# Optimization experiments

Measured on AMD Instinct MI355X. Metric: run time of the kernel, lower is better.

The kernel has to match this reference:

```python
import jax, jax.numpy as jnp
import numpy as np

NUM_HEADS = 6
H_SP, W_SP = 8, 16
LN_EPS = 1e-5


def _ln(x, g, b):
    m = x.mean(-1, keepdims=True)
    v = ((x - m) ** 2).mean(-1, keepdims=True)
    return (x - m) / jnp.sqrt(v + LN_EPS) * g + b


def setup_inputs():
    key = jax.random.key(0)
    ks = jax.random.split(key, 8)
    B, H, W, C = 8, 128, 128, 192
    L = H * W
    N = H_SP * W_SP
    nW = L // N
    pos_dim = C // 16  # (dim//4)//4 = 12
    qkv = jax.random.normal(ks[0], (3, B, L, C), jnp.float32)
    mask = jax.random.normal(ks[1], (nW, N, N), jnp.float32) * 0.1

    def lin(k, i, o):
        return jax.random.normal(k, (i, o), jnp.float32) * 0.02

    pos_dimv = pos_dim
    pos_proj_w = lin(ks[2], 2, pos_dimv); pos_proj_b = jnp.zeros((pos_dimv,), jnp.float32)
    ln1_g = jnp.ones((pos_dimv,), jnp.float32); ln1_b = jnp.zeros((pos_dimv,), jnp.float32)
    lin1_w = lin(ks[3], pos_dimv, pos_dimv); lin1_b = jnp.zeros((pos_dimv,), jnp.float32)
    ln2_g = jnp.ones((pos_dimv,), jnp.float32); ln2_b = jnp.zeros((pos_dimv,), jnp.float32)
    lin2_w = lin(ks[4], pos_dimv, pos_dimv); lin2_b = jnp.zeros((pos_dimv,), jnp.float32)
    ln3_g = jnp.ones((pos_dimv,), jnp.float32); ln3_b = jnp.zeros((pos_dimv,), jnp.float32)
    lin3_w = lin(ks[5], pos_dimv, NUM_HEADS); lin3_b = jnp.zeros((NUM_HEADS,), jnp.float32)
    # buffers: rpe_biases [(2Hsp-1)*(2Wsp-1), 2], relative_position_index [N, N]
    ph = np.arange(1 - H_SP, H_SP); pw = np.arange(1 - W_SP, W_SP)
    biases = np.stack(np.meshgrid(ph, pw, indexing='ij')).reshape(2, -1).T.astype(np.float32)
    coords = np.stack(np.meshgrid(np.arange(H_SP), np.arange(W_SP), indexing='ij')).reshape(2, -1)
    rel = (coords[:, :, None] - coords[:, None, :]).transpose(1, 2, 0).copy()
    rel[..., 0] += H_SP - 1
    rel[..., 1] += W_SP - 1
    rel[..., 0] *= 2 * W_SP - 1
    rel_idx = rel.sum(-1).astype(np.int32)
    return dict(qkv=qkv, mask=mask, pos_proj_w=pos_proj_w, pos_proj_b=pos_proj_b,
                ln1_g=ln1_g, ln1_b=ln1_b, lin1_w=lin1_w, lin1_b=lin1_b,
                ln2_g=ln2_g, ln2_b=ln2_b, lin2_w=lin2_w, lin2_b=lin2_b,
                ln3_g=ln3_g, ln3_b=ln3_b, lin3_w=lin3_w, lin3_b=lin3_b,
                rpe_biases=jnp.asarray(biases), rel_idx=jnp.asarray(rel_idx), H=H, W=W)


def reference(qkv, mask, pos_proj_w, pos_proj_b, ln1_g, ln1_b, lin1_w, lin1_b,
              ln2_g, ln2_b, lin2_w, lin2_b, ln3_g, ln3_b, lin3_w, lin3_b,
              rpe_biases, rel_idx, H, W):
    q, k, v = qkv[0], qkv[1], qkv[2]
    B, L, C = q.shape
    hd = C // NUM_HEADS
    scale = hd ** -0.5
    N = H_SP * W_SP
    nW = H * W // N
    # pooled query: adaptive avg-pool on first half channels, max-pool on second half
    q_img = q.transpose(0, 2, 1).reshape(B, C, H, W)
    half = C // 2
    blocks = lambda t: t.reshape(B, -1, H_SP, H // H_SP, W_SP, W // W_SP)
    q1 = blocks(q_img[:, :half]).mean(axis=(3, 5))   # [B, C/2, Hsp, Wsp]
    q2 = blocks(q_img[:, half:]).max(axis=(3, 5))
    qp = jnp.concatenate([q1, q2], 1).reshape(B, NUM_HEADS, hd, N).transpose(0, 1, 3, 2)
    qw = jnp.tile(qp, (nW, 1, 1, 1)) * scale  # [B*nW, h, N, d]  (torch .repeat ordering)

    def im2win(x):  # [B, L, C] -> [B*nW, h, N, d]
        xi = x.transpose(0, 2, 1).reshape(B, C, H // H_SP, H_SP, W // W_SP, W_SP)
        xi = xi.transpose(0, 2, 4, 3, 5, 1).reshape(-1, N, C)
        return xi.reshape(-1, N, NUM_HEADS, hd).transpose(0, 2, 1, 3)

    kw, vw = im2win(k), im2win(v)
    attn = jnp.einsum('whqd,whkd->whqk', qw, kw)  # [B*nW, h, N, N]
    # DynamicPosBias MLP on relative coordinates, gathered into scores
    pos = rpe_biases @ pos_proj_w + pos_proj_b
    pos = jax.nn.relu(_ln(pos, ln1_g, ln1_b)) @ lin1_w + lin1_b
    pos = jax.nn.relu(_ln(pos, ln2_g, ln2_b)) @ lin2_w + lin2_b
    pos = jax.nn.relu(_ln(pos, ln3_g, ln3_b)) @ lin3_w + lin3_b  # [M, heads]
    rpb = pos[rel_idx]  # [N, N, heads]
    attn = attn + rpb.transpose(2, 0, 1)[None]
    attn = attn.reshape(B, nW, NUM_HEADS, N, N) + mask[None, :, None]
    attn = jax.nn.softmax(attn.reshape(-1, NUM_HEADS, N, N), axis=-1)
    x = jnp.einsum('whqk,whkd->whqd', attn, vw).transpose(0, 2, 1, 3).reshape(-1, N, C)
    # windows2img
    out = x.reshape(B, H // H_SP, W // W_SP, H_SP, W_SP, C)
    out = out.transpose(0, 1, 3, 2, 4, 5).reshape(B, H, W, C)
    return out
```

## Files before the change

kernel.cpp:

```cpp
#include <hip/hip_runtime.h>
#include <cstdint>
#include <cstddef>

typedef __attribute__((ext_vector_type(8))) short short8;
typedef __attribute__((ext_vector_type(4))) float f32x4;

#define SCALE 0.17677669529663687f
#define KOFF 25165824UL
#define VOFF 50331648UL

__device__ __forceinline__ float bf2f(unsigned short u){
  union { unsigned int i; float f; } x; x.i = ((unsigned int)u) << 16; return x.f;
}
__device__ __forceinline__ unsigned short f2bf(float f){
  union { float f; unsigned int i; } x; x.f = f;
  unsigned int u = x.i;
  unsigned int r = u + 0x7fffu + ((u >> 16) & 1u);
  return (unsigned short)(r >> 16);
}

__device__ __forceinline__ int detect_bf16(const void* probe){
  const unsigned short* p = (const unsigned short*)probe;
  int ok = 1;
  #pragma unroll
  for (int i = 0; i < 32; i++){
    unsigned short u = p[2*i];
    int e = (u >> 7) & 0xFF;
    ok &= (e >= 0x60 && e <= 0x90) ? 1 : 0;
  }
  return ok;
}

__device__ __forceinline__ float ld1(const void* p, size_t i, int isbf){
  return isbf ? bf2f(((const unsigned short*)p)[i]) : ((const float*)p)[i];
}
__device__ __forceinline__ short8 ld8(const void* p, size_t i, int isbf){
  short8 r;
  if (isbf){
    r = *(const short8*)((const unsigned short*)p + i);
  } else {
    const float4* f = (const float4*)((const float*)p + i);
    float4 u0 = f[0], u1 = f[1];
    r[0] = (short)f2bf(u0.x); r[1] = (short)f2bf(u0.y);
    r[2] = (short)f2bf(u0.z); r[3] = (short)f2bf(u0.w);
    r[4] = (short)f2bf(u1.x); r[5] = (short)f2bf(u1.y);
    r[6] = (short)f2bf(u1.z); r[7] = (short)f2bf(u1.w);
  }
  return r;
}
__device__ __forceinline__ float4 ld4(const void* p, size_t i, int isbf){
  if (!isbf) return *(const float4*)((const float*)p + i);
  const unsigned short* u = (const unsigned short*)p + i;
  uint2 w = *(const uint2*)u;
  float4 r;
  r.x = bf2f((unsigned short)(w.x & 0xffffu)); r.y = bf2f((unsigned short)(w.x >> 16));
  r.z = bf2f((unsigned short)(w.y & 0xffffu)); r.w = bf2f((unsigned short)(w.y >> 16));
  return r;
}

__global__ void posmlp_kernel(const void* __restrict__ probe,
    const void* __restrict__ rpe,
    const void* __restrict__ w0, const void* __restrict__ b0,
    const void* __restrict__ g1, const void* __restrict__ be1,
    const void* __restrict__ w1, const void* __restrict__ bb1,
    const void* __restrict__ g2, const void* __restrict__ be2,
    const void* __restrict__ w2, const void* __restrict__ bb2,
    const void* __restrict__ g3, const void* __restrict__ be3,
    const void* __restrict__ w3, const void* __restrict__ bb3,
    float* __restrict__ pos_table)
{
  const int isbf = detect_bf16(probe);
  int r = blockIdx.x * blockDim.x + threadIdx.x;
  if (r >= 465) return;
  float x0 = ld1(rpe, 2*r, isbf), x1 = ld1(rpe, 2*r+1, isbf);
  float h[12], y[12];
  #pragma unroll
  for (int j=0;j<12;j++) h[j] = x0*ld1(w0,j,isbf) + x1*ld1(w0,12+j,isbf) + ld1(b0,j,isbf);

  {
    float m=0.f;
    #pragma unroll
    for (int j=0;j<12;j++) m += h[j];
    m *= (1.f/12.f);
    float v=0.f;
    #pragma unroll
    for (int j=0;j<12;j++){ float d=h[j]-m; v += d*d; }
    v *= (1.f/12.f);
    float rs = 1.0f/sqrtf(v + 1e-5f);
    #pragma unroll
    for (int j=0;j<12;j++) y[j] = fmaxf((h[j]-m)*rs*ld1(g1,j,isbf) + ld1(be1,j,isbf), 0.f);
    #pragma unroll
    for (int j=0;j<12;j++){
      float s = ld1(bb1,j,isbf);
      #pragma unroll
      for (int i=0;i<12;i++) s += y[i]*ld1(w1,i*12+j,isbf);
      h[j] = s;
    }
  }
  {
    float m=0.f;
    #pragma unroll
    for (int j=0;j<12;j++) m += h[j];
    m *= (1.f/12.f);
    float v=0.f;
    #pragma unroll
    for (int j=0;j<12;j++){ float d=h[j]-m; v += d*d; }
    v *= (1.f/12.f);
    float rs = 1.0f/sqrtf(v + 1e-5f);
    #pragma unroll
    for (int j=0;j<12;j++) y[j] = fmaxf((h[j]-m)*rs*ld1(g2,j,isbf) + ld1(be2,j,isbf), 0.f);
    #pragma unroll
    for (int j=0;j<12;j++){
      float s = ld1(bb2,j,isbf);
      #pragma unroll
      for (int i=0;i<12;i++) s += y[i]*ld1(w2,i*12+j,isbf);
      h[j] = s;
    }
  }
  {
    float m=0.f;
    #pragma unroll
    for (int j=0;j<12;j++) m += h[j];
    m *= (1.f/12.f);
    float v=0.f;
    #pragma unroll
    for (int j=0;j<12;j++){ float d=h[j]-m; v += d*d; }
    v *= (1.f/12.f);
    float rs = 1.0f/sqrtf(v + 1e-5f);
    #pragma unroll
    for (int j=0;j<12;j++) y[j] = fmaxf((h[j]-m)*rs*ld1(g3,j,isbf) + ld1(be3,j,isbf), 0.f);
    #pragma unroll
    for (int o=0;o<6;o++){
      float s = ld1(bb3,o,isbf);
      #pragma unroll
      for (int i=0;i<12;i++) s += y[i]*ld1(w3,i*6+o,isbf);
      pos_table[r*6+o] = s;
    }
  }
}

__global__ void gatherN_kernel(const int* __restrict__ rel_idx,
                               const float* __restrict__ pos_table,
                               unsigned short* __restrict__ rpbN)
{
  const int idx = blockIdx.x * 256 + threadIdx.x;
  const int h = blockIdx.y;
  rpbN[h*16384 + idx] = f2bf(pos_table[rel_idx[idx]*6 + h]);
}

__global__ void pool_kernel(const void* __restrict__ qkv,
                            unsigned short* __restrict__ poolq)
{
  const int isbf = detect_bf16(qkv);
  const int b = blockIdx.y;
  const int n = blockIdx.x;
  const int t = threadIdx.x;
  const int cg = t % 48, sub = t / 48;
  const int ph = n >> 4, pw = n & 15;
  const size_t cell = ((size_t)(b*16384 + ph*16*128 + pw*8))*192 + cg*4;
  const bool avg = (cg < 24);
  float4 acc;
  if (avg){ acc.x=0.f; acc.y=0.f; acc.z=0.f; acc.w=0.f; }
  else    { acc.x=-3.4e38f; acc.y=-3.4e38f; acc.z=-3.4e38f; acc.w=-3.4e38f; }
  #pragma unroll
  for (int hh=0; hh<4; hh++){
    const int hi = sub*4 + hh;
    #pragma unroll
    for (int wi=0; wi<8; wi++){
      float4 xv = ld4(qkv, cell + (size_t)(hi*128 + wi)*192, isbf);
      if (avg){ acc.x+=xv.x; acc.y+=xv.y; acc.z+=xv.z; acc.w+=xv.w; }
      else { acc.x=fmaxf(acc.x,xv.x); acc.y=fmaxf(acc.y,xv.y);
             acc.z=fmaxf(acc.z,xv.z); acc.w=fmaxf(acc.w,xv.w); }
    }
  }
  __shared__ float4 pr[4][48];
  pr[sub][cg] = acc;
  __syncthreads();
  if (sub == 0){
    #pragma unroll
    for (int s=1; s<4; s++){
      float4 xv = pr[s][cg];
      if (avg){ acc.x+=xv.x; acc.y+=xv.y; acc.z+=xv.z; acc.w+=xv.w; }
      else { acc.x=fmaxf(acc.x,xv.x); acc.y=fmaxf(acc.y,xv.y);
             acc.z=fmaxf(acc.z,xv.z); acc.w=fmaxf(acc.w,xv.w); }
    }
    if (avg){ acc.x*=(1.f/128.f); acc.y*=(1.f/128.f); acc.z*=(1.f/128.f); acc.w*=(1.f/128.f); }
    unsigned int lo = (unsigned int)f2bf(acc.x*SCALE) | ((unsigned int)f2bf(acc.y*SCALE) << 16);
    unsigned int hi = (unsigned int)f2bf(acc.z*SCALE) | ((unsigned int)f2bf(acc.w*SCALE) << 16);
    uint2 st; st.x = lo; st.y = hi;
    *(uint2*)(poolq + ((size_t)b*128 + n)*192 + cg*4) = st;
  }
}

__global__ __launch_bounds__(256, 4)
void attn_kernel(const void* __restrict__ qkv,
                 const unsigned short* __restrict__ poolq,
                 const void* __restrict__ mask,
                 const unsigned short* __restrict__ rpbN,
                 void* __restrict__ out)
{
  const int isbf = detect_bf16(qkv);
  const int iw = blockIdx.x, b = blockIdx.y, head = blockIdx.z;
  const int hb = iw >> 3, wb = iw & 7;
  const int qb = iw & 7;
  const int tid = threadIdx.x;
  const int lane = tid & 63, wv = tid >> 6;
  const int quad = lane >> 4, c16 = lane & 15;

  __shared__ unsigned short Kt[128][40];
  __shared__ unsigned short Vt[32][136];

  {
    const int tok = tid >> 1;
    const int dh  = (tid & 1) << 4;
    const size_t rowidx = ((size_t)((b*128 + hb*8 + (tok>>4))*128 + wb*16 + (tok&15)))*192 + head*32 + dh;
    short8 k0 = ld8(qkv, KOFF + rowidx, isbf);
    short8 k1 = ld8(qkv, KOFF + rowidx + 8, isbf);
    *(short8*)(&Kt[tok][dh])     = k0;
    *(short8*)(&Kt[tok][dh + 8]) = k1;
    short8 v0 = ld8(qkv, VOFF + rowidx, isbf);
    short8 v1 = ld8(qkv, VOFF + rowidx + 8, isbf);
    const int t5 = tok & 31;
    const int stok = (tok & ~31) | (((t5>>2)&3)*8) | (((t5>>4)&1)*4) | (t5&3);
    #pragma unroll
    for (int u=0; u<8; u++){
      Vt[dh + u][stok]     = (unsigned short)v0[u];
      Vt[dh + 8 + u][stok] = (unsigned short)v1[u];
    }
  }

  short8 qf[2];
  #pragma unroll
  for (int tm=0; tm<2; tm++)
    qf[tm] = *(const short8*)(poolq + ((size_t)(qb*128 + (wv*2+tm)*16 + c16))*192 + head*32 + quad*8);

  __syncthreads();

  f32x4 acc[8][2];
  const size_t mbase = (size_t)iw*16384;
  const size_t rbase = (size_t)head*16384;
  #pragma unroll
  for (int tn=0; tn<8; tn++){
    short8 kA = *(const short8*)(&Kt[tn*16 + c16][quad*8]);
    f32x4 z = {0.f, 0.f, 0.f, 0.f};
    acc[tn][0] = __builtin_amdgcn_mfma_f32_16x16x32_bf16(kA, qf[0], z, 0, 0, 0);
    acc[tn][1] = __builtin_amdgcn_mfma_f32_16x16x32_bf16(kA, qf[1], z, 0, 0, 0);
    const int nb = tn*16 + quad*4;
    #pragma unroll
    for (int tm=0; tm<2; tm++){
      const int m = wv*32 + tm*16 + c16;
      float4 mv = ld4(mask, mbase + (size_t)m*128 + nb, isbf);
      uint2 rv = *(const uint2*)(rpbN + rbase + (size_t)m*128 + nb);
      acc[tn][tm][0] += mv.x + bf2f((unsigned short)(rv.x & 0xffffu));
      acc[tn][tm][1] += mv.y + bf2f((unsigned short)(rv.x >> 16));
      acc[tn][tm][2] += mv.z + bf2f((unsigned short)(rv.y & 0xffffu));
      acc[tn][tm][3] += mv.w + bf2f((unsigned short)(rv.y >> 16));
    }
  }

  float wsc[2];
  short8 pa[4][2];
  #pragma unroll
  for (int tm=0; tm<2; tm++){
    float mx = acc[0][tm][0];
    #pragma unroll
    for (int tn=0; tn<8; tn++)
      #pragma unroll
      for (int r=0; r<4; r++) mx = fmaxf(mx, acc[tn][tm][r]);
    mx = fmaxf(mx, __shfl_xor(mx, 16));
    mx = fmaxf(mx, __shfl_xor(mx, 32));
    float s = 0.f;
    #pragma unroll
    for (int tn=0; tn<8; tn++)
      #pragma unroll
      for (int r=0; r<4; r++){
        float p = __expf(acc[tn][tm][r] - mx);
        acc[tn][tm][r] = p;
        s += p;
      }
    s += __shfl_xor(s, 16);
    s += __shfl_xor(s, 32);
    wsc[tm] = 1.0f / s;
    #pragma unroll
    for (int jt=0; jt<4; jt++)
      #pragma unroll
      for (int u=0; u<8; u++)
        pa[jt][tm][u] = (short)(__float_as_uint(acc[2*jt + (u>>2)][tm][u & 3]) >> 16);
  }

  f32x4 o[2][2];
  #pragma unroll
  for (int tm=0; tm<2; tm++)
    #pragma unroll
    for (int dt=0; dt<2; dt++){ f32x4 z = {0.f,0.f,0.f,0.f}; o[tm][dt] = z; }
  #pragma unroll
  for (int jt=0; jt<4; jt++){
    short8 vA0 = *(const short8*)&Vt[c16][jt*32 + quad*8];
    short8 vA1 = *(const short8*)&Vt[16 + c16][jt*32 + quad*8];
    o[0][0] = __builtin_amdgcn_mfma_f32_16x16x32_bf16(vA0, pa[jt][0], o[0][0], 0, 0, 0);
    o[0][1] = __builtin_amdgcn_mfma_f32_16x16x32_bf16(vA1, pa[jt][0], o[0][1], 0, 0, 0);
    o[1][0] = __builtin_amdgcn_mfma_f32_16x16x32_bf16(vA0, pa[jt][1], o[1][0], 0, 0, 0);
    o[1][1] = __builtin_amdgcn_mfma_f32_16x16x32_bf16(vA1, pa[jt][1], o[1][1], 0, 0, 0);
  }

  #pragma unroll
  for (int tm=0; tm<2; tm++){
    const int m = wv*32 + tm*16 + c16;
    const int hh = hb*8 + (m >> 4), ww = wb*16 + (m & 15);
    const size_t obase = ((size_t)((b*128 + hh)*128 + ww))*192 + head*32;
    #pragma unroll
    for (int dt=0; dt<2; dt++){
      float4 val;
      val.x = o[tm][dt][0] * wsc[tm];
      val.y = o[tm][dt][1] * wsc[tm];
      val.z = o[tm][dt][2] * wsc[tm];
      val.w = o[tm][dt][3] * wsc[tm];
      const size_t off = obase + dt*16 + quad*4;
      if (isbf){
        unsigned int lo = (unsigned int)f2bf(val.x) | ((unsigned int)f2bf(val.y) << 16);
        unsigned int hi = (unsigned int)f2bf(val.z) | ((unsigned int)f2bf(val.w) << 16);
        uint2 st; st.x = lo; st.y = hi;
        *(uint2*)((unsigned short*)out + off) = st;
      } else {
        *(float4*)((float*)out + off) = val;
      }
    }
  }
}

extern "C" void kernel_launch(void* const* d_in, const int* in_sizes, int n_in,
                              void* d_out, int out_size, void* d_ws, size_t ws_size,
                              hipStream_t stream)
{
  const void* qkv  = d_in[0];
  const void* mask = d_in[1];
  const int* rel_idx = (const int*)d_in[17];

  float* pos_table     = (float*)d_ws;
  unsigned short* rpbN = (unsigned short*)((char*)d_ws + 12288);
  unsigned short* poolq= (unsigned short*)((char*)d_ws + 12288 + 196608);

  posmlp_kernel<<<1, 512, 0, stream>>>(qkv, d_in[16],
      d_in[2], d_in[3], d_in[4], d_in[5], d_in[6], d_in[7],
      d_in[8], d_in[9], d_in[10], d_in[11], d_in[12], d_in[13],
      d_in[14], d_in[15], pos_table);
  gatherN_kernel<<<dim3(64, 6), 256, 0, stream>>>(rel_idx, pos_table, rpbN);
  pool_kernel<<<dim3(128, 8), 192, 0, stream>>>(qkv, poolq);
  attn_kernel<<<dim3(128, 8, 6), 256, 0, stream>>>(qkv, poolq, mask, rpbN, d_out);
}
```

Before: 780.6 us.

## Pre-permute relative position bias to fragment layout and stage output through LDS

Result: no change. 776.1 us (-0.6%).

```diff
diff --git a/kernel.cpp b/kernel.cpp
--- a/kernel.cpp
+++ b/kernel.cpp
@@ -139,13 +139,22 @@
   }
 }
 
-__global__ void gatherN_kernel(const int* __restrict__ rel_idx,
+__global__ void gatherP_kernel(const int* __restrict__ rel_idx,
                                const float* __restrict__ pos_table,
-                               unsigned short* __restrict__ rpbN)
-{
-  const int idx = blockIdx.x * 256 + threadIdx.x;
-  const int h = blockIdx.y;
-  rpbN[h*16384 + idx] = f2bf(pos_table[rel_idx[idx]*6 + h]);
+                               unsigned short* __restrict__ rpbP)
+{
+  const int t = blockIdx.x * 256 + threadIdx.x;
+  const int tm = t & 1, lane = (t >> 1) & 63, wv = (t >> 7) & 3, tn = (t >> 9) & 7, h = t >> 12;
+  const int c16 = lane & 15, quad = lane >> 4;
+  const int m = wv*32 + tm*16 + c16;
+  const int nb = tn*16 + quad*4;
+  const int* ri = rel_idx + m*128 + nb;
+  unsigned int lo = (unsigned int)f2bf(pos_table[ri[0]*6 + h])
+                  | ((unsigned int)f2bf(pos_table[ri[1]*6 + h]) << 16);
+  unsigned int hi = (unsigned int)f2bf(pos_table[ri[2]*6 + h])
+                  | ((unsigned int)f2bf(pos_table[ri[3]*6 + h]) << 16);
+  uint2 st; st.x = lo; st.y = hi;
+  *(uint2*)(rpbP + ((size_t)((h*8 + tn)*4 + wv)*64 + lane)*8 + tm*4) = st;
 }
 
 __global__ void pool_kernel(const void* __restrict__ qkv,
@@ -196,7 +205,7 @@
 void attn_kernel(const void* __restrict__ qkv,
                  const unsigned short* __restrict__ poolq,
                  const void* __restrict__ mask,
-                 const unsigned short* __restrict__ rpbN,
+                 const unsigned short* __restrict__ rpbP,
                  void* __restrict__ out)
 {
   const int isbf = detect_bf16(qkv);
@@ -207,8 +216,21 @@
   const int lane = tid & 63, wv = tid >> 6;
   const int quad = lane >> 4, c16 = lane & 15;
 
-  __shared__ unsigned short Kt[128][40];
-  __shared__ unsigned short Vt[32][136];
+  __shared__ __align__(16) unsigned char lds_raw[18944];
+  unsigned short (*Kt)[40]  = (unsigned short (*)[40])lds_raw;
+  unsigned short (*Vt)[136] = (unsigned short (*)[136])(lds_raw + 10240);
+
+  short8 qf[2];
+  #pragma unroll
+  for (int tm=0; tm<2; tm++)
+    qf[tm] = *(const short8*)(poolq + ((size_t)(qb*128 + (wv*2+tm)*16 + c16))*192 + head*32 + quad*8);
+  uint4 rfr[8];
+  {
+    const unsigned short* rb = rpbP + (size_t)head*16384;
+    #pragma unroll
+    for (int tn=0; tn<8; tn++)
+      rfr[tn] = *(const uint4*)(rb + (size_t)((tn*4 + wv)*64 + lane)*8);
+  }
 
   {
     const int tok = tid >> 1;
@@ -229,16 +251,10 @@
     }
   }
 
-  short8 qf[2];
-  #pragma unroll
-  for (int tm=0; tm<2; tm++)
-    qf[tm] = *(const short8*)(poolq + ((size_t)(qb*128 + (wv*2+tm)*16 + c16))*192 + head*32 + quad*8);
-
   __syncthreads();
 
   f32x4 acc[8][2];
   const size_t mbase = (size_t)iw*16384;
-  const size_t rbase = (size_t)head*16384;
   #pragma unroll
   for (int tn=0; tn<8; tn++){
     short8 kA = *(const short8*)(&Kt[tn*16 + c16][quad*8]);
@@ -246,15 +262,22 @@
     acc[tn][0] = __builtin_amdgcn_mfma_f32_16x16x32_bf16(kA, qf[0], z, 0, 0, 0);
     acc[tn][1] = __builtin_amdgcn_mfma_f32_16x16x32_bf16(kA, qf[1], z, 0, 0, 0);
     const int nb = tn*16 + quad*4;
-    #pragma unroll
-    for (int tm=0; tm<2; tm++){
-      const int m = wv*32 + tm*16 + c16;
+    const uint4 rv = rfr[tn];
+    {
+      const int m = wv*32 + c16;
       float4 mv = ld4(mask, mbase + (size_t)m*128 + nb, isbf);
-      uint2 rv = *(const uint2*)(rpbN + rbase + (size_t)m*128 + nb);
-      acc[tn][tm][0] += mv.x + bf2f((unsigned short)(rv.x & 0xffffu));
-      acc[tn][tm][1] += mv.y + bf2f((unsigned short)(rv.x >> 16));
-      acc[tn][tm][2] += mv.z + bf2f((unsigned short)(rv.y & 0xffffu));
-      acc[tn][tm][3] += mv.w + bf2f((unsigned short)(rv.y >> 16));
+      acc[tn][0][0] += mv.x + bf2f((unsigned short)(rv.x & 0xffffu));
+      acc[tn][0][1] += mv.y + bf2f((unsigned short)(rv.x >> 16));
+      acc[tn][0][2] += mv.z + bf2f((unsigned short)(rv.y & 0xffffu));
+      acc[tn][0][3] += mv.w + bf2f((unsigned short)(rv.y >> 16));
+    }
+    {
+      const int m = wv*32 + 16 + c16;
+      float4 mv = ld4(mask, mbase + (size_t)m*128 + nb, isbf);
+      acc[tn][1][0] += mv.x + bf2f((unsigned short)(rv.z & 0xffffu));
+      acc[tn][1][1] += mv.y + bf2f((unsigned short)(rv.z >> 16));
+      acc[tn][1][2] += mv.z + bf2f((unsigned short)(rv.w & 0xffffu));
+      acc[tn][1][3] += mv.w + bf2f((unsigned short)(rv.w >> 16));
     }
   }
 
@@ -303,26 +326,32 @@
     o[1][1] = __builtin_amdgcn_mfma_f32_16x16x32_bf16(vA1, pa[jt][1], o[1][1], 0, 0, 0);
   }
 
-  #pragma unroll
-  for (int tm=0; tm<2; tm++){
-    const int m = wv*32 + tm*16 + c16;
-    const int hh = hb*8 + (m >> 4), ww = wb*16 + (m & 15);
-    const size_t obase = ((size_t)((b*128 + hh)*128 + ww))*192 + head*32;
-    #pragma unroll
-    for (int dt=0; dt<2; dt++){
-      float4 val;
-      val.x = o[tm][dt][0] * wsc[tm];
-      val.y = o[tm][dt][1] * wsc[tm];
-      val.z = o[tm][dt][2] * wsc[tm];
-      val.w = o[tm][dt][3] * wsc[tm];
-      const size_t off = obase + dt*16 + quad*4;
+  __syncthreads();
+
+  float* w = (float*)lds_raw + wv*1152;
+  #pragma unroll
+  for (int tm=0; tm<2; tm++)
+    #pragma unroll
+    for (int dt=0; dt<2; dt++)
+      #pragma unroll
+      for (int r=0; r<4; r++)
+        w[(tm*16 + c16)*36 + dt*16 + quad*4 + r] = o[tm][dt][r] * wsc[tm];
+  {
+    const int tk = lane >> 1;
+    const int h2 = lane & 1;
+    const int token = wv*32 + tk;
+    const int hh = hb*8 + (token >> 4), ww = wb*16 + (token & 15);
+    const size_t obase = ((size_t)((b*128 + hh)*128 + ww))*192 + head*32 + h2*16;
+    #pragma unroll
+    for (int it=0; it<4; it++){
+      float4 val = *(const float4*)&w[tk*36 + h2*16 + it*4];
       if (isbf){
         unsigned int lo = (unsigned int)f2bf(val.x) | ((unsigned int)f2bf(val.y) << 16);
         unsigned int hi = (unsigned int)f2bf(val.z) | ((unsigned int)f2bf(val.w) << 16);
         uint2 st; st.x = lo; st.y = hi;
-        *(uint2*)((unsigned short*)out + off) = st;
+        *(uint2*)((unsigned short*)out + obase + it*4) = st;
       } else {
-        *(float4*)((float*)out + off) = val;
+        *(float4*)((float*)out + obase + it*4) = val;
       }
     }
   }
@@ -336,15 +365,15 @@
   const void* mask = d_in[1];
   const int* rel_idx = (const int*)d_in[17];
 
-  float* pos_table     = (float*)d_ws;
-  unsigned short* rpbN = (unsigned short*)((char*)d_ws + 12288);
-  unsigned short* poolq= (unsigned short*)((char*)d_ws + 12288 + 196608);
+  float* pos_table      = (float*)d_ws;
+  unsigned short* rpbP  = (unsigned short*)((char*)d_ws + 12288);
+  unsigned short* poolq = (unsigned short*)((char*)d_ws + 208896);
 
   posmlp_kernel<<<1, 512, 0, stream>>>(qkv, d_in[16],
       d_in[2], d_in[3], d_in[4], d_in[5], d_in[6], d_in[7],
       d_in[8], d_in[9], d_in[10], d_in[11], d_in[12], d_in[13],
       d_in[14], d_in[15], pos_table);
-  gatherN_kernel<<<dim3(64, 6), 256, 0, stream>>>(rel_idx, pos_table, rpbN);
+  gatherP_kernel<<<96, 256, 0, stream>>>(rel_idx, pos_table, rpbP);
   pool_kernel<<<dim3(128, 8), 192, 0, stream>>>(qkv, poolq);
-  attn_kernel<<<dim3(128, 8, 6), 256, 0, stream>>>(qkv, poolq, mask, rpbN, d_out);
-}
+  attn_kernel<<<dim3(128, 8, 6), 256, 0, stream>>>(qkv, poolq, mask, rpbP, d_out);
+}
```
